# Optimization experiments

Measured on AMD Instinct MI355X. Metric: run time of the kernel, lower is better.

The kernel has to match this reference:

```python
import jax, jax.numpy as jnp
import numpy as np
import math


def setup_inputs() -> dict:
    B, L, D, P, V = 4, 4096, 512, 128, 8
    key = jax.random.key(0)
    ki = iter(jax.random.split(key, 40))
    def rn(shape, s=0.02):
        return jax.random.normal(next(ki), shape, jnp.float32) * s
    z = lambda *s: jnp.zeros(s, jnp.float32)
    return dict(
        x=jax.random.normal(next(ki), (B, L, D), jnp.float32),
        W_omega=rn((D, D)), b_omega=z(D),
        omega_scale=jnp.full((D,), 0.01, jnp.float32),
        W_pi1=rn((D, D)), b_pi1=z(D), W_pi2=rn((D, D)), b_pi2=z(D),
        W_m1v=rn((D, D)), b_m1v=z(D),
        W_m1o=rn((D, D)), b_m1o=z(D),
        W_mag=rn((D, D)), b_mag=z(D),
        mag_scale=jnp.asarray(5.0, jnp.float32),
        W_qoff=rn((D, D)), b_qoff=z(D),
        W_kenc=rn((D, P)), b_kenc=z(P),
        W_venc=rn((D, V)), b_venc=z(V),
        W_sk1=rn((2 * D, D)), b_sk1=z(D),
        W_sk2=rn((D, P)), b_sk2=z(P),
        W_sg=rn((D, 1)), b_sg=z(1),
        W_kvo=rn((V, D)), b_kvo=z(D),
        ln_g=jnp.ones((4 * D,), jnp.float32), ln_b=z(4 * D),
        W_o1=rn((4 * D, 2 * D)), b_o1=z(2 * D),
        W_o2=rn((2 * D, D)), b_o2=z(D),
    )


def _lin(h, W, b):
    return h @ W + b


def _gelu(h):
    return jax.nn.gelu(h, approximate=False)  # torch nn.GELU default (erf)


def _forward(x, W_omega, b_omega, omega_scale, W_pi1, b_pi1, W_pi2, b_pi2,
             W_m1v, b_m1v, W_m1o, b_m1o, W_mag, b_mag, mag_scale,
             W_qoff, b_qoff, W_kenc, b_kenc, W_venc, b_venc,
             W_sk1, b_sk1, W_sk2, b_sk2, W_sg, b_sg, W_kvo, b_kvo,
             ln_g, ln_b, W_o1, b_o1, W_o2, b_o2):
    B, L, D = x.shape
    P = W_kenc.shape[1]
    # --- evolving phases ---
    omega_scaled = _lin(x, W_omega, b_omega) * jnp.abs(omega_scale)
    phi_init = _lin(_gelu(_lin(x, W_pi1, b_pi1)), W_pi2, b_pi2)
    phi = phi_init + jnp.cumsum(omega_scaled, axis=1)
    cos_phi, sin_phi = jnp.cos(phi), jnp.sin(phi)
    # --- memory 1: positional phasor memory ---
    v1 = _lin(x, W_m1v, b_m1v)
    magnitude = jax.nn.sigmoid(_lin(x, W_mag, b_mag)) * jnp.abs(mag_scale)
    wv1 = magnitude * v1
    sqrt_mag = jnp.sqrt(jnp.cumsum(magnitude, axis=1) + 1e-8)
    mem1_cos = jnp.cumsum(wv1 * cos_phi, axis=1) / sqrt_mag
    mem1_sin = jnp.cumsum(wv1 * sin_phi, axis=1) / sqrt_mag
    phi_q = phi + _lin(x, W_qoff, b_qoff)
    pos_ret = (mem1_cos * jnp.cos(phi_q) + mem1_sin * jnp.sin(phi_q)) / math.sqrt(D)
    pos_out = _lin(pos_ret, W_m1o, b_m1o)
    # --- memory 2: key/value phasor binding ---
    query_phase = jnp.tanh(_lin(x, W_kenc, b_kenc)) * math.pi
    values = _lin(x, W_venc, b_venc)                      # [B,L,V]
    store_gate = jax.nn.sigmoid(_lin(x, W_sg, b_sg))      # [B,L,1]
    positions = jnp.arange(1, L + 1, dtype=x.dtype)[None, :, None]
    context_avg = jnp.cumsum(x, axis=1) / positions
    sk_in = jnp.concatenate([x, context_avg], axis=-1)
    storage_phase = jnp.tanh(_lin(_gelu(_lin(sk_in, W_sk1, b_sk1)), W_sk2, b_sk2)) * math.pi
    store_cos, store_sin = jnp.cos(storage_phase), jnp.sin(storage_phase)  # [B,L,P]
    gv = values * store_gate                               # [B,L,V]
    # [B,L,P,V] outer products, cumsum along L
    kv_mem_cos = jnp.cumsum(store_cos[..., None] * gv[:, :, None, :], axis=1)
    kv_mem_sin = jnp.cumsum(store_sin[..., None] * gv[:, :, None, :], axis=1)
    gate_cum = jnp.clip(jnp.cumsum(store_gate, axis=1), 1.0, None)  # [B,L,1]
    inv_norm = (1.0 / jnp.sqrt(gate_cum))[..., None]
    kv_mem_cos = kv_mem_cos * inv_norm
    kv_mem_sin = kv_mem_sin * inv_norm
    q_cos, q_sin = jnp.cos(query_phase), jnp.sin(query_phase)
    kv_retrieved = (jnp.einsum('blp,blpv->blv', q_cos, kv_mem_cos)
                    + jnp.einsum('blp,blpv->blv', q_sin, kv_mem_sin)) / math.sqrt(P)
    kv_out = _lin(kv_retrieved, W_kvo, b_kvo)
    # --- output projection ---
    combined = jnp.concatenate([pos_out, kv_out, x * cos_phi, x * sin_phi], axis=-1)
    mu = combined.mean(axis=-1, keepdims=True)
    var = combined.var(axis=-1, keepdims=True)
    h = (combined - mu) / jnp.sqrt(var + 1e-5) * ln_g + ln_b
    h = _gelu(_lin(h, W_o1, b_o1))  # dropout is identity in eval mode
    return x + _lin(h, W_o2, b_o2)


def reference(x, W_omega, b_omega, omega_scale, W_pi1, b_pi1, W_pi2, b_pi2,
              W_m1v, b_m1v, W_m1o, b_m1o, W_mag, b_mag, mag_scale,
              W_qoff, b_qoff, W_kenc, b_kenc, W_venc, b_venc,
              W_sk1, b_sk1, W_sk2, b_sk2, W_sg, b_sg, W_kvo, b_kvo,
              ln_g, ln_b, W_o1, b_o1, W_o2, b_o2):
    return _forward(x, W_omega, b_omega, omega_scale, W_pi1, b_pi1, W_pi2, b_pi2,
                    W_m1v, b_m1v, W_m1o, b_m1o, W_mag, b_mag, mag_scale,
                    W_qoff, b_qoff, W_kenc, b_kenc, W_venc, b_venc,
                    W_sk1, b_sk1, W_sk2, b_sk2, W_sg, b_sg, W_kvo, b_kvo,
                    ln_g, ln_b, W_o1, b_o1, W_o2, b_o2)
```

## Files before the change

### kernel.cpp

```cpp
#include <hip/hip_runtime.h>
#include <math.h>

#define B_ 4
#define L_ 4096
#define D_ 512
#define P_ 128
#define V_ 8
#define N_ (B_*L_)
#define NC 64
#define CL (L_/NC)
#define LD ((size_t)L_*D_)
#define PI_F 3.14159265358979323846f

typedef unsigned short ushort;
typedef __attribute__((ext_vector_type(8))) short bh8;
typedef __attribute__((ext_vector_type(4))) float f4;
typedef const __attribute__((address_space(1))) unsigned int gu32;
typedef __attribute__((address_space(3))) unsigned int lu32;

__device__ __forceinline__ float geluf(float v){
    return 0.5f*v*(1.0f+erff(v*0.7071067811865475f));
}
__device__ __forceinline__ float tanhf_fast(float x){
    return 1.0f - 2.0f/(__expf(2.0f*x)+1.0f);
}
__device__ __forceinline__ ushort f2b(float f){
    union { float f; unsigned u; } v; v.f = f;
    unsigned r = (v.u + 0x7fffu + ((v.u >> 16) & 1u)) >> 16;
    return (ushort)r;
}
__device__ __forceinline__ float b2f(ushort h){
    union { unsigned u; float f; } v; v.u = ((unsigned)h) << 16;
    return v.f;
}
__device__ __forceinline__ void gload16(const ushort* g, ushort* l){
    __builtin_amdgcn_global_load_lds((gu32*)g, (lu32*)l, 16, 0, 0);
}
__device__ __forceinline__ int xcd_swz(int orig, int nwg){
    int q8 = nwg >> 3, r8 = nwg & 7;
    int xcd = orig & 7, sub = orig >> 3;
    return (xcd < r8 ? xcd*(q8+1) : r8*(q8+1) + (xcd-r8)*q8) + sub;
}

template<int ACT>
__global__ __launch_bounds__(256, 2)
void dgemm_k(const ushort* __restrict__ A, int lda,
             const ushort* __restrict__ Wt, const float* __restrict__ bias,
             ushort* __restrict__ Ob, float* __restrict__ Of,
             int ldc, int K, const float* __restrict__ addbuf)
{
    __shared__ ushort lA[2][128*64];
    __shared__ ushort lB[2][128*64];
    const int tid = threadIdx.x, lane = tid & 63, w = tid >> 6;
    const int wr = w >> 1, wc = w & 1;
    const int nbx = gridDim.x;
    const int wg = xcd_swz(blockIdx.y*nbx + blockIdx.x, nbx*gridDim.y);
    const int row0 = (wg / nbx) * 128, col0 = (wg % nbx) * 128;

    f4 zero4 = {0.f,0.f,0.f,0.f};
    f4 acc[4][4];
    #pragma unroll
    for (int i=0;i<4;i++)
        #pragma unroll
        for (int j=0;j<4;j++) acc[i][j] = zero4;

    auto stage = [&](int buf, int kt){
        #pragma unroll
        for (int is=0; is<4; ++is){
            int id = tid + is*256;
            int r = id >> 3, p = id & 7;
            int srcc = (p ^ (r & 7)) * 8;
            gload16(A + (size_t)(row0 + r)*lda + kt + srcc, &lA[buf][r*64 + p*8]);
        }
        #pragma unroll
        for (int is=0; is<4; ++is){
            int id = tid + is*256;
            int r = id >> 3, p = id & 7;
            int srcc = (p ^ (r & 7)) * 8;
            gload16(Wt + (size_t)(col0 + r)*K + kt + srcc, &lB[buf][r*64 + p*8]);
        }
    };

    const int NT = K >> 6;
    stage(0, 0);
    for (int t2 = 0; t2 < NT; ++t2){
        int cur = t2 & 1;
        if (t2 + 1 < NT){
            stage(cur ^ 1, (t2+1) << 6);
            asm volatile("s_waitcnt vmcnt(8)" ::: "memory");
        } else {
            asm volatile("s_waitcnt vmcnt(0)" ::: "memory");
        }
        __builtin_amdgcn_s_barrier();
        __builtin_amdgcn_sched_barrier(0);
        #pragma unroll
        for (int h=0; h<2; ++h){
            bh8 af[4], bf_[4];
            #pragma unroll
            for (int i=0;i<4;i++){
                int row = wr*64 + i*16 + (lane & 15);
                int pc = (h*4 + (lane >> 4)) ^ (row & 7);
                af[i] = *(const bh8*)&lA[cur][row*64 + pc*8];
            }
            #pragma unroll
            for (int j=0;j<4;j++){
                int row = wc*64 + j*16 + (lane & 15);
                int pc = (h*4 + (lane >> 4)) ^ (row & 7);
                bf_[j] = *(const bh8*)&lB[cur][row*64 + pc*8];
            }
            #pragma unroll
            for (int i=0;i<4;i++)
                #pragma unroll
                for (int j=0;j<4;j++)
                    acc[i][j] = __builtin_amdgcn_mfma_f32_16x16x32_bf16(af[i], bf_[j], acc[i][j], 0, 0, 0);
        }
        __builtin_amdgcn_sched_barrier(0);
        __builtin_amdgcn_s_barrier();
    }

    #pragma unroll
    for (int i=0;i<4;i++){
        int rr = row0 + wr*64 + i*16 + ((lane >> 4) << 2);
        #pragma unroll
        for (int j=0;j<4;j++){
            int cc = col0 + wc*64 + j*16 + (lane & 15);
            float bv = bias[cc];
            #pragma unroll
            for (int q=0;q<4;q++){
                int r = rr + q;
                float t = acc[i][j][q] + bv;
                if (ACT==2){
                    if (addbuf) t += addbuf[(size_t)r*512 + cc];
                    Of[(size_t)r*ldc + cc] = t;
                } else {
                    if (ACT==1) t = geluf(t);
                    Ob[(size_t)r*ldc + cc] = f2b(t);
                }
            }
        }
    }
}

__global__ __launch_bounds__(256, 2)
void fgemm_k(const ushort* __restrict__ A, int lda, const ushort* __restrict__ Wt,
             const float* __restrict__ bs0, const float* __restrict__ bs1,
             const float* __restrict__ bs2, const float* __restrict__ bs3,
             const float* __restrict__ bs4, const float* __restrict__ bs5,
             ushort* __restrict__ o0, ushort* __restrict__ o1p, ushort* __restrict__ o2p,
             ushort* __restrict__ o3p, ushort* __restrict__ o4p,
             ushort* __restrict__ Qc, ushort* __restrict__ Qs,
             const float* __restrict__ omsc, const float* __restrict__ magscp, int K)
{
    __shared__ ushort lA[2][128*32];
    __shared__ ushort lB[2][128*32];
    const int tid = threadIdx.x, lane = tid & 63, w = tid >> 6;
    const int wr = w >> 1, wc = w & 1;
    const int nbx = gridDim.x;
    const int wg = xcd_swz(blockIdx.y*nbx + blockIdx.x, nbx*gridDim.y);
    const int row0 = (wg / nbx) * 128, col0 = (wg % nbx) * 128;

    const int srow = w*32 + (lane >> 2);
    const int sch  = lane & 3;
    const int scolA = (sch ^ (srow & 3)) * 8;
    const ushort* gA0 = A  + (size_t)(row0 + srow)      * lda + scolA;
    const ushort* gA1 = A  + (size_t)(row0 + srow + 16) * lda + scolA;
    const ushort* gB0 = Wt + (size_t)(col0 + srow)      * K   + scolA;
    const ushort* gB1 = Wt + (size_t)(col0 + srow + 16) * K   + scolA;
    const int d0 = srow*32 + sch*8, d1 = (srow+16)*32 + sch*8;

    f4 zero4 = {0.f,0.f,0.f,0.f};
    f4 acc[4][4];
    #pragma unroll
    for (int i=0;i<4;i++)
        #pragma unroll
        for (int j=0;j<4;j++) acc[i][j] = zero4;

    const int fr = lane & 15;
    const int pcr = (((lane >> 4) ^ (fr & 3))) * 8;
    gload16(gA0, &lA[0][d0]); gload16(gA1, &lA[0][d1]);
    gload16(gB0, &lB[0][d0]); gload16(gB1, &lB[0][d1]);
    __syncthreads();
    int cur = 0;
    for (int kt = 0; kt < K; kt += 32) {
        int nxt = cur ^ 1;
        if (kt + 32 < K) {
            gload16(gA0 + kt + 32, &lA[nxt][d0]); gload16(gA1 + kt + 32, &lA[nxt][d1]);
            gload16(gB0 + kt + 32, &lB[nxt][d0]); gload16(gB1 + kt + 32, &lB[nxt][d1]);
        }
        bh8 af[4], bfr[4];
        #pragma unroll
        for (int i=0;i<4;i++){
            af[i]  = *(const bh8*)&lA[cur][(wr*64 + i*16 + fr)*32 + pcr];
            bfr[i] = *(const bh8*)&lB[cur][(wc*64 + i*16 + fr)*32 + pcr];
        }
        #pragma unroll
        for (int i=0;i<4;i++)
            #pragma unroll
            for (int j=0;j<4;j++)
                acc[i][j] = __builtin_amdgcn_mfma_f32_16x16x32_bf16(af[i], bfr[j], acc[i][j], 0, 0, 0);
        __syncthreads();
        cur = nxt;
    }

    const int seg = col0 >> 9;
    if (seg == 5) {
        #pragma unroll
        for (int i=0;i<4;i++){
            int rr = row0 + wr*64 + i*16 + ((lane >> 4) << 2);
            #pragma unroll
            for (int j=0;j<4;j++){
                int lcc = (col0 - 2560) + wc*64 + j*16 + (lane & 15);
                float bv = bs5[lcc];
                #pragma unroll
                for (int q=0;q<4;q++){
                    int r = rr + q;
                    float ph = tanhf_fast(acc[i][j][q] + bv)*PI_F;
                    Qc[(size_t)r*128 + lcc] = f2b(__cosf(ph));
                    Qs[(size_t)r*128 + lcc] = f2b(__sinf(ph));
                }
            }
        }
        return;
    }
    const float* bias = seg==0?bs0: seg==1?bs1: seg==2?bs2: seg==3?bs3: bs4;
    ushort* dst = seg==0?o0: seg==1?o1p: seg==2?o2p: seg==3?o3p: o4p;
    float msc = fabsf(*magscp);
    #pragma unroll
    for (int i=0;i<4;i++){
        int rr = row0 + wr*64 + i*16 + ((lane >> 4) << 2);
        #pragma unroll
        for (int j=0;j<4;j++){
            int cc = col0 + wc*64 + j*16 + (lane & 15);
            int lcc = cc & 511;
            float bv = bias[lcc];
            float csc = (seg==0) ? fabsf(omsc[lcc]) : 1.0f;
            #pragma unroll
            for (int q=0;q<4;q++){
                int r = rr + q;
                float t = acc[i][j][q] + bv;
                if (seg==1)      t = msc/(1.0f+__expf(-t));
                else if (seg==3) t = geluf(t);
                else             t *= csc;
                dst[(size_t)r*512 + lcc] = f2b(t);
            }
        }
    }
}

__global__ __launch_bounds__(256, 2)
void mgemm_k(const ushort* __restrict__ Apos, const ushort* __restrict__ Ask,
             const ushort* __restrict__ Wm1o, const ushort* __restrict__ Wsk2,
             const float* __restrict__ bm1o, const float* __restrict__ bsk2,
             ushort* __restrict__ planes, ushort* __restrict__ Kc, ushort* __restrict__ Ks)
{
    __shared__ ushort lA[2][128*32];
    __shared__ ushort lB[2][128*32];
    const int tid = threadIdx.x, lane = tid & 63, w = tid >> 6;
    const int wr = w >> 1, wc = w & 1;
    const int nbx = gridDim.x;
    const int wg = xcd_swz(blockIdx.y*nbx + blockIdx.x, nbx*gridDim.y);
    const int row0 = (wg / nbx) * 128, col0 = (wg % nbx) * 128;
    const int seg = col0 >> 9;
    const ushort* A  = seg ? Ask  : Apos;
    const ushort* Wt = seg ? Wsk2 : Wm1o;
    const int wcol0 = seg ? (col0 - 512) : col0;
    const int K = 512;

    const int srow = w*32 + (lane >> 2);
    const int sch  = lane & 3;
    const int scolA = (sch ^ (srow & 3)) * 8;
    const ushort* gA0 = A  + (size_t)(row0 + srow)       * 512 + scolA;
    const ushort* gA1 = A  + (size_t)(row0 + srow + 16)  * 512 + scolA;
    const ushort* gB0 = Wt + (size_t)(wcol0 + srow)      * 512 + scolA;
    const ushort* gB1 = Wt + (size_t)(wcol0 + srow + 16) * 512 + scolA;
    const int d0 = srow*32 + sch*8, d1 = (srow+16)*32 + sch*8;

    f4 zero4 = {0.f,0.f,0.f,0.f};
    f4 acc[4][4];
    #pragma unroll
    for (int i=0;i<4;i++)
        #pragma unroll
        for (int j=0;j<4;j++) acc[i][j] = zero4;

    const int fr = lane & 15;
    const int pcr = (((lane >> 4) ^ (fr & 3))) * 8;
    gload16(gA0, &lA[0][d0]); gload16(gA1, &lA[0][d1]);
    gload16(gB0, &lB[0][d0]); gload16(gB1, &lB[0][d1]);
    __syncthreads();
    int cur = 0;
    for (int kt = 0; kt < K; kt += 32) {
        int nxt = cur ^ 1;
        if (kt + 32 < K) {
            gload16(gA0 + kt + 32, &lA[nxt][d0]); gload16(gA1 + kt + 32, &lA[nxt][d1]);
            gload16(gB0 + kt + 32, &lB[nxt][d0]); gload16(gB1 + kt + 32, &lB[nxt][d1]);
        }
        bh8 af[4], bfr[4];
        #pragma unroll
        for (int i=0;i<4;i++){
            af[i]  = *(const bh8*)&lA[cur][(wr*64 + i*16 + fr)*32 + pcr];
            bfr[i] = *(const bh8*)&lB[cur][(wc*64 + i*16 + fr)*32 + pcr];
        }
        #pragma unroll
        for (int i=0;i<4;i++)
            #pragma unroll
            for (int j=0;j<4;j++)
                acc[i][j] = __builtin_amdgcn_mfma_f32_16x16x32_bf16(af[i], bfr[j], acc[i][j], 0, 0, 0);
        __syncthreads();
        cur = nxt;
    }

    #pragma unroll
    for (int i=0;i<4;i++){
        int rr = row0 + wr*64 + i*16 + ((lane >> 4) << 2);
        #pragma unroll
        for (int j=0;j<4;j++){
            int cc = col0 + wc*64 + j*16 + (lane & 15);
            #pragma unroll
            for (int q=0;q<4;q++){
                int r = rr + q;
                if (seg == 0){
                    planes[(size_t)r*2048 + cc] = f2b(acc[i][j][q] + bm1o[cc]);
                } else {
                    int lcc = cc - 512;
                    float ph = tanhf_fast(acc[i][j][q] + bsk2[lcc])*PI_F;
                    Kc[(size_t)r*128 + lcc] = f2b(__cosf(ph));
                    Ks[(size_t)r*128 + lcc] = f2b(__sinf(ph));
                }
            }
        }
    }
}

struct WtArgs {
    const float* src[12];
    ushort* dst[12];
    int K[12], M[12], t0[13];
};
__global__ __launch_bounds__(256)
void wtall_k(WtArgs a)
{
    __shared__ float tile[32][33];
    int bb = blockIdx.x;
    int j = 0;
    while (bb >= a.t0[j+1]) ++j;
    int tt = bb - a.t0[j];
    int K = a.K[j], M = a.M[j];
    int mt = M >> 5;
    int kb = (tt / mt) * 32, mb = (tt % mt) * 32;
    const float* W = a.src[j]; ushort* Wt = a.dst[j];
    int tx = threadIdx.x & 31, ty = threadIdx.x >> 5;
    #pragma unroll
    for (int i = ty; i < 32; i += 8)
        tile[i][tx] = W[(size_t)(kb+i)*M + mb+tx];
    __syncthreads();
    #pragma unroll
    for (int i = ty; i < 32; i += 8)
        Wt[(size_t)(mb+i)*K + kb+tx] = f2b(tile[tx][i]);
}

__global__ __launch_bounds__(256)
void fconv_k(const float* __restrict__ in, ushort* __restrict__ xctx)
{
    size_t i = ((size_t)blockIdx.x*256 + threadIdx.x) * 4;
    size_t row = i >> 9; int d = (int)(i & 511);
    float4 v = *(const float4*)(in + i);
    ushort* o = xctx + row*1024 + d;
    o[0]=f2b(v.x); o[1]=f2b(v.y); o[2]=f2b(v.z); o[3]=f2b(v.w);
}

__global__ __launch_bounds__(256)
void s1a_k(const ushort* __restrict__ omega, const ushort* __restrict__ xctx,
           float* __restrict__ csA, float* __restrict__ csX)
{
    int bid = blockIdx.x;
    int b = bid >> 7; int rem = bid & 127;
    int dg = rem & 1, c = rem >> 1;
    int d = dg*256 + threadIdx.x;
    size_t row0 = (size_t)b*L_ + (size_t)c*CL;
    size_t base = row0*D_ + d;
    float sA=0.f, sX=0.f;
    for (int l=0;l<CL;l++){
        sA += b2f(omega[base + (size_t)l*D_]);
        sX += b2f(xctx[(row0 + l)*1024 + d]);
    }
    size_t ci = ((size_t)b*NC + c)*D_ + d;
    csA[ci]=sA; csX[ci]=sX;
}

__global__ __launch_bounds__(256)
void aux1_k(float* __restrict__ csA, float* __restrict__ csX,
            const float* __restrict__ sgate, float* __restrict__ rinv, int nb2)
{
    __shared__ float wsum[4];
    __shared__ float carry;
    int bb = blockIdx.x, t = threadIdx.x;
    if (bb < nb2){
        int tt = bb*256 + t;
        int b = tt >> 9, d = tt & 511;
        float* bufs[2] = {csA, csX};
        #pragma unroll
        for (int i=0;i<2;i++){
            float* p = bufs[i] + ((size_t)b*NC)*D_ + d;
            float run=0.f;
            for (int c=0;c<NC;c++){
                float v = p[(size_t)c*D_];
                p[(size_t)c*D_] = run;
                run += v;
            }
        }
        return;
    }
    int b = bb - nb2;
    int lane = t & 63, wave = t >> 6;
    if (t == 0) carry = 0.f;
    __syncthreads();
    for (int s = 0; s < L_/256; s++){
        float v = sgate[(size_t)b*L_ + s*256 + t];
        float sc = v;
        #pragma unroll
        for (int off=1; off<64; off<<=1){
            float u = __shfl_up(sc, off, 64);
            if (lane >= off) sc += u;
        }
        if (lane == 63) wsum[wave] = sc;
        __syncthreads();
        float woff = carry;
        for (int w2 = 0; w2 < wave; w2++) woff += wsum[w2];
        float inc = sc + woff;
        rinv[(size_t)b*L_ + s*256 + t] = rsqrtf(fmaxf(inc, 1.0f));
        __syncthreads();
        if (t == 255) carry = inc;
        __syncthreads();
    }
}

__global__ void prefix_k(float* a, float* b2v, float* c3, int nbuf)
{
    int t = blockIdx.x*blockDim.x + threadIdx.x;
    int b = t >> 9, d = t & 511;
    float* bufs[3] = {a,b2v,c3};
    for (int i=0;i<nbuf;i++){
        float* p = bufs[i] + ((size_t)b*NC)*D_ + d;
        float run=0.f;
        for (int c=0;c<NC;c++){
            float v = p[(size_t)c*D_];
            p[(size_t)c*D_] = run;
            run += v;
        }
    }
}

__global__ __launch_bounds__(256)
void s1c_k(const ushort* __restrict__ omega, const ushort* __restrict__ phi_init,
           const ushort* __restrict__ magn, const ushort* __restrict__ v1,
           const float* __restrict__ csA, const float* __restrict__ csX,
           ushort* __restrict__ cphi, ushort* __restrict__ sphi, ushort* __restrict__ xctx,
           float* __restrict__ csM, float* __restrict__ csC, float* __restrict__ csS)
{
    int bid = blockIdx.x;
    int b = bid >> 7; int rem = bid & 127;
    int dg = rem & 1, c = rem >> 1;
    int d = dg*256 + threadIdx.x;
    size_t ci = ((size_t)b*NC + c)*D_ + d;
    float phiacc = csA[ci], xacc = csX[ci];
    float sM=0.f,sC=0.f,sS=0.f;
    size_t xrow = (size_t)b*L_ + (size_t)c*CL;
    size_t base = xrow*D_ + d;
    for (int l=0;l<CL;l++){
        size_t idx = base + (size_t)l*D_;
        phiacc += b2f(omega[idx]);
        float ph = b2f(phi_init[idx]) + phiacc;
        float spv = __sinf(ph), cpv = __cosf(ph);
        cphi[idx] = f2b(cpv); sphi[idx] = f2b(spv);
        xacc += b2f(xctx[(xrow + l)*1024 + d]);
        xctx[(xrow + l)*1024 + 512 + d] = f2b(__fdividef(xacc, (float)(c*CL + l + 1)));
        float m = b2f(magn[idx]); sM += m;
        float wv = m * b2f(v1[idx]);
        sC = fmaf(wv, cpv, sC); sS = fmaf(wv, spv, sS);
    }
    csM[ci]=sM; csC[ci]=sC; csS[ci]=sS;
}

__global__ __launch_bounds__(256)
void s1e_k(const ushort* __restrict__ magn, const ushort* __restrict__ v1,
           const ushort* qoff, const ushort* __restrict__ cphi, const ushort* __restrict__ sphi,
           const float* __restrict__ csM, const float* __restrict__ csC,
           const float* __restrict__ csS, ushort* pos_ret)
{
    int bid = blockIdx.x;
    int b = bid >> 7; int rem = bid & 127;
    int dg = rem & 1, c = rem >> 1;
    int d = dg*256 + threadIdx.x;
    size_t ci = ((size_t)b*NC + c)*D_ + d;
    float mA=csM[ci], cA=csC[ci], sA=csS[ci];
    size_t base = ((size_t)b*L_ + (size_t)c*CL)*D_ + d;
    for (int l=0;l<CL;l++){
        size_t idx = base + (size_t)l*D_;
        float m = b2f(magn[idx]); mA += m;
        float wv = m * b2f(v1[idx]);
        float cp = b2f(cphi[idx]), sp = b2f(sphi[idx]);
        cA = fmaf(wv, cp, cA); sA = fmaf(wv, sp, sA);
        float rs = rsqrtf(mA + 1e-8f);
        float qo = b2f(qoff[idx]);
        float sq = __sinf(qo), cq = __cosf(qo);
        float cosq = cp*cq - sp*sq;
        float sinq = sp*cq + cp*sq;
        pos_ret[idx] = f2b((cA*cosq + sA*sinq) * rs * 0.04419417382415922f);
    }
}

__global__ __launch_bounds__(256)
void vencsg_k(const ushort* __restrict__ xctx, const float* __restrict__ Wv,
              const float* __restrict__ bv, const float* __restrict__ Wg,
              const float* __restrict__ bg,
              ushort* __restrict__ gvb, float* __restrict__ sgate)
{
    int gw = (int)((blockIdx.x*(size_t)blockDim.x + threadIdx.x) >> 6);
    int lane = threadIdx.x & 63;
    const ushort* xr = xctx + (size_t)gw*1024;
    float pv[8] = {0,0,0,0,0,0,0,0}; float pg = 0.f;
    #pragma unroll
    for (int j=0;j<8;j++){
        int k = lane + 64*j;
        float xv = b2f(xr[k]);
        #pragma unroll
        for (int v=0;v<8;v++) pv[v] = fmaf(xv, Wv[k*8+v], pv[v]);
        pg = fmaf(xv, Wg[k], pg);
    }
    #pragma unroll
    for (int off=32; off>0; off>>=1){
        #pragma unroll
        for (int v=0;v<8;v++) pv[v] += __shfl_down(pv[v], off, 64);
        pg += __shfl_down(pg, off, 64);
    }
    if (lane==0){
        float sg = 1.0f/(1.0f+__expf(-(pg + bg[0])));
        #pragma unroll
        for (int v=0;v<8;v++) gvb[(size_t)gw*8+v] = f2b((pv[v] + bv[v]) * sg);
        sgate[gw] = sg;
    }
}

__global__ __launch_bounds__(256)
void kvsum_k(const ushort* __restrict__ Kc, const ushort* __restrict__ Ks,
             const ushort* __restrict__ gvb, float* __restrict__ csKV)
{
    int bid = blockIdx.x;
    int b = bid >> 6, c = bid & 63;
    int t = threadIdx.x; int p = t & 127; int v0 = (t>>7)*4;
    size_t row0 = (size_t)b*L_ + (size_t)c*64;
    float ac[4]={0,0,0,0}, as[4]={0,0,0,0};
    for (int l=0;l<64;l++){
        size_t r = row0 + l;
        float kc = b2f(Kc[r*(size_t)P_ + p]);
        float ks = b2f(Ks[r*(size_t)P_ + p]);
        #pragma unroll
        for (int j=0;j<4;j++){
            float gv = b2f(gvb[r*(size_t)V_ + v0 + j]);
            ac[j] = fmaf(kc, gv, ac[j]);
            as[j] = fmaf(ks, gv, as[j]);
        }
    }
    float* base = csKV + ((size_t)b*64 + c)*2048;
    #pragma unroll
    for (int j=0;j<4;j++){
        base[p*V_ + v0 + j] = ac[j];
        base[1024 + p*V_ + v0 + j] = as[j];
    }
}

__global__ void kvpfx_k(float* __restrict__ csKV)
{
    int t = blockIdx.x*blockDim.x + threadIdx.x;
    int b = t >> 11, si = t & 2047;
    float* ptr = csKV + ((size_t)b*64)*2048 + si;
    float run=0.f;
    for (int c=0;c<64;c++){
        float v = ptr[(size_t)c*2048];
        ptr[(size_t)c*2048] = run;
        run += v;
    }
}

__global__ __launch_bounds__(256)
void kv2_k(const ushort* __restrict__ Qc, const ushort* __restrict__ Qs,
           const ushort* __restrict__ Kc, const ushort* __restrict__ Ks,
           const ushort* __restrict__ gvb, const float* __restrict__ rinv,
           const float* __restrict__ csKV, float* __restrict__ kvret)
{
    __shared__ ushort sS[64][66];
    __shared__ float sM[2048];
    __shared__ float sgv[64][8];
    int tile = blockIdx.x, b = blockIdx.y;
    int t = threadIdx.x, lane = t & 63, w = t >> 6;
    int wr = w >> 1, wc = w & 1;
    size_t row0 = (size_t)b*L_ + (size_t)tile*64;
    const float* kvb = csKV + ((size_t)b*64 + tile)*2048;
    #pragma unroll
    for (int k=0;k<8;k++) sM[t + k*256] = kvb[t + k*256];
    #pragma unroll
    for (int k=0;k<2;k++){
        int idx = t + k*256; int l = idx >> 3, v = idx & 7;
        sgv[l][v] = b2f(gvb[(row0 + l)*(size_t)V_ + v]);
    }
    f4 zero4 = {0.f,0.f,0.f,0.f};
    f4 acc[2][2];
    #pragma unroll
    for (int i=0;i<2;i++)
        #pragma unroll
        for (int j=0;j<2;j++) acc[i][j] = zero4;
    #pragma unroll
    for (int ks=0; ks<8; ks++){
        const ushort* Ab = (ks<4) ? Qc : Qs;
        const ushort* Bb = (ks<4) ? Kc : Ks;
        int kb = (ks&3)*32 + (lane>>4)*8;
        bh8 af[2], bfr[2];
        #pragma unroll
        for (int i=0;i<2;i++)
            af[i] = *(const bh8*)(Ab + (row0 + wr*32 + i*16 + (lane&15))*(size_t)P_ + kb);
        #pragma unroll
        for (int j=0;j<2;j++)
            bfr[j] = *(const bh8*)(Bb + (row0 + wc*32 + j*16 + (lane&15))*(size_t)P_ + kb);
        #pragma unroll
        for (int i=0;i<2;i++)
            #pragma unroll
            for (int j=0;j<2;j++)
                acc[i][j] = __builtin_amdgcn_mfma_f32_16x16x32_bf16(af[i], bfr[j], acc[i][j], 0, 0, 0);
    }
    #pragma unroll
    for (int i=0;i<2;i++){
        #pragma unroll
        for (int j=0;j<2;j++){
            int cc = wc*32 + j*16 + (lane & 15);
            #pragma unroll
            for (int q=0;q<4;q++){
                int lr = wr*32 + i*16 + ((lane>>4)<<2) + q;
                sS[lr][cc] = f2b((cc <= lr) ? acc[i][j][q] : 0.f);
            }
        }
    }
    __syncthreads();
    int l = t & 63, vh = t >> 6; int v0 = vh*2;
    const ushort* qcr = Qc + (row0 + l)*(size_t)P_;
    const ushort* qsr = Qs + (row0 + l)*(size_t)P_;
    float a0=0.f, a1=0.f;
    #pragma unroll
    for (int pc=0; pc<16; pc++){
        bh8 qc8 = *(const bh8*)(qcr + pc*8);
        bh8 qs8 = *(const bh8*)(qsr + pc*8);
        #pragma unroll
        for (int e=0;e<8;e++){
            int p = pc*8+e;
            float qc = b2f((ushort)qc8[e]), qs = b2f((ushort)qs8[e]);
            a0 += qc*sM[p*8+v0]   + qs*sM[1024+p*8+v0];
            a1 += qc*sM[p*8+v0+1] + qs*sM[1024+p*8+v0+1];
        }
    }
    for (int c=0;c<64;c++){
        float sv = b2f(sS[l][c]);
        a0 = fmaf(sv, sgv[c][v0],   a0);
        a1 = fmaf(sv, sgv[c][v0+1], a1);
    }
    float rn = rinv[row0 + l] * 0.08838834764831845f;
    kvret[(row0+l)*(size_t)V_ + v0]   = a0*rn;
    kvret[(row0+l)*(size_t)V_ + v0+1] = a1*rn;
}

__global__ __launch_bounds__(256)
void cmb_k(const ushort* __restrict__ xctx, const ushort* __restrict__ cphi,
           const ushort* __restrict__ sphi,
           const float* __restrict__ kvret, const float* __restrict__ Wkvo,
           const float* __restrict__ bkvo,
           const float* __restrict__ ln_g, const float* __restrict__ ln_b,
           ushort* pl)
{
    __shared__ float red[8];
    __shared__ float kvv[8];
    int n = blockIdx.x; int t = threadIdx.x;
    int wave = t>>6, lane = t&63;
    if (t < 8) kvv[t] = kvret[(size_t)n*8 + t];
    __syncthreads();
    float v_[8]; float sum=0.f, sumsq=0.f;
    #pragma unroll
    for (int i=0;i<8;i++){
        int cidx = t + i*256;
        int seg = cidx >> 9, cc = cidx & 511;
        float v;
        if (seg == 0) v = b2f(pl[(size_t)n*2048 + cidx]);
        else if (seg == 1) {
            v = bkvo[cc];
            #pragma unroll
            for (int vv=0; vv<8; vv++) v = fmaf(kvv[vv], Wkvo[vv*512 + cc], v);
        } else {
            size_t id = (size_t)n*D_ + cc;
            v = b2f(xctx[(size_t)n*1024 + cc]) * b2f((seg==2) ? cphi[id] : sphi[id]);
        }
        v_[i]=v; sum += v; sumsq = fmaf(v,v,sumsq);
    }
    #pragma unroll
    for (int off=32; off>0; off>>=1){
        sum += __shfl_xor(sum, off, 64);
        sumsq += __shfl_xor(sumsq, off, 64);
    }
    if (lane==0){ red[wave]=sum; red[wave+4]=sumsq; }
    __syncthreads();
    float s = red[0]+red[1]+red[2]+red[3];
    float q = red[4]+red[5]+red[6]+red[7];
    float mu = s * (1.0f/2048.0f);
    float var = q * (1.0f/2048.0f) - mu*mu;
    float rstd = rsqrtf(var + 1e-5f);
    #pragma unroll
    for (int i=0;i<8;i++){
        int cidx = t + i*256;
        float h = (v_[i]-mu)*rstd*ln_g[cidx] + ln_b[cidx];
        pl[(size_t)n*2048 + cidx] = f2b(h);
    }
}

__global__ void copyx_k(const float* __restrict__ x, float* __restrict__ out, size_t n)
{
    size_t i = (size_t)blockIdx.x*256 + threadIdx.x;
    if (i < n) out[i] = x[i];
}

struct WS {
    ushort *wt_fused,*wt_pi2,*wt_sk1,*wt_sk2,*wt_m1o,*wt_o1,*wt_o2;
    ushort *xctx, *pool;
    ushort *Qc,*Qs,*Kc,*Ks,*gvb,*cphi,*sphi;
    float *sgate,*rinv,*kvret;
    float *csA,*csX,*csM,*csC,*csS,*csKV;
};

static size_t ws_layout(WS& w, char* base, int NB)
{
    size_t off = 0;
    auto al = [&](size_t bytes)->char* {
        char* p = base + off; off = (off + bytes + 255) & ~(size_t)255; return p;
    };
    size_t R = (size_t)NB * L_;
    w.wt_fused=(ushort*)al((size_t)2688*512*2);
    w.wt_pi2 =(ushort*)al(512*512*2);
    w.wt_sk1 =(ushort*)al((size_t)512*1024*2); w.wt_sk2=(ushort*)al(128*512*2);
    w.wt_m1o =(ushort*)al(512*512*2);
    w.wt_o1  =(ushort*)al((size_t)1024*2048*2); w.wt_o2=(ushort*)al((size_t)512*1024*2);
    w.xctx=(ushort*)al(R*1024*2);
    w.pool=(ushort*)al(R*512*2*6);
    w.Qc=(ushort*)al(R*128*2); w.Qs=(ushort*)al(R*128*2);
    w.Kc=(ushort*)al(R*128*2); w.Ks=(ushort*)al(R*128*2);
    w.gvb=(ushort*)al(R*8*2);
    w.cphi=(ushort*)al(R*512*2); w.sphi=(ushort*)al(R*512*2);
    w.sgate=(float*)al(R*4); w.rinv=(float*)al(R*4); w.kvret=(float*)al(R*8*4);
    w.csA=(float*)al((size_t)NB*NC*512*4); w.csX=(float*)al((size_t)NB*NC*512*4);
    w.csM=(float*)al((size_t)NB*NC*512*4); w.csC=(float*)al((size_t)NB*NC*512*4);
    w.csS=(float*)al((size_t)NB*NC*512*4);
    w.csKV=(float*)al((size_t)NB*64*2048*4);
    return off;
}

extern "C" void kernel_launch(void* const* d_in, const int* in_sizes, int n_in,
                              void* d_out, int out_size, void* d_ws, size_t ws_size,
                              hipStream_t stream)
{
    const float* x        =(const float*)d_in[0];
    const float* W_omega  =(const float*)d_in[1];  const float* b_omega=(const float*)d_in[2];
    const float* omega_sc =(const float*)d_in[3];
    const float* W_pi1    =(const float*)d_in[4];  const float* b_pi1 =(const float*)d_in[5];
    const float* W_pi2    =(const float*)d_in[6];  const float* b_pi2 =(const float*)d_in[7];
    const float* W_m1v    =(const float*)d_in[8];  const float* b_m1v =(const float*)d_in[9];
    const float* W_m1o    =(const float*)d_in[10]; const float* b_m1o =(const float*)d_in[11];
    const float* W_mag    =(const float*)d_in[12]; const float* b_mag =(const float*)d_in[13];
    const float* mag_sc   =(const float*)d_in[14];
    const float* W_qoff   =(const float*)d_in[15]; const float* b_qoff=(const float*)d_in[16];
    const float* W_kenc   =(const float*)d_in[17]; const float* b_kenc=(const float*)d_in[18];
    const float* W_venc   =(const float*)d_in[19]; const float* b_venc=(const float*)d_in[20];
    const float* W_sk1    =(const float*)d_in[21]; const float* b_sk1 =(const float*)d_in[22];
    const float* W_sk2    =(const float*)d_in[23]; const float* b_sk2 =(const float*)d_in[24];
    const float* W_sg     =(const float*)d_in[25]; const float* b_sg  =(const float*)d_in[26];
    const float* W_kvo    =(const float*)d_in[27]; const float* b_kvo =(const float*)d_in[28];
    const float* ln_g     =(const float*)d_in[29]; const float* ln_b  =(const float*)d_in[30];
    const float* W_o1     =(const float*)d_in[31]; const float* b_o1  =(const float*)d_in[32];
    const float* W_o2     =(const float*)d_in[33]; const float* b_o2  =(const float*)d_in[34];
    float* out = (float*)d_out;

    char* wsb = (char*)d_ws;
    WS w;
    int NB = 4;
    if (ws_layout(w, wsb, 4) > ws_size) {
        NB = 2;
        if (ws_layout(w, wsb, 2) > ws_size) {
            NB = 1;
            if (ws_layout(w, wsb, 1) > ws_size) {
                copyx_k<<<dim3((unsigned)(((size_t)N_*D_ + 255)/256)), dim3(256), 0, stream>>>(x, out, (size_t)N_*D_);
                return;
            }
        }
    }

    dim3 blk(256);
    WtArgs wa;
    const float* srcs[12] = {W_omega, W_mag, W_m1v, W_pi1, W_qoff, W_kenc,
                             W_pi2, W_sk1, W_sk2, W_m1o, W_o1, W_o2};
    ushort* dsts[12] = {w.wt_fused + (size_t)0*512*512, w.wt_fused + (size_t)1*512*512,
                        w.wt_fused + (size_t)2*512*512, w.wt_fused + (size_t)3*512*512,
                        w.wt_fused + (size_t)4*512*512, w.wt_fused + (size_t)5*512*512,
                        w.wt_pi2, w.wt_sk1, w.wt_sk2, w.wt_m1o, w.wt_o1, w.wt_o2};
    int Ks_[12] = {512,512,512,512,512,512, 512,1024,512,512,2048,1024};
    int Ms_[12] = {512,512,512,512,512,128, 512, 512,128,512,1024, 512};
    int cum = 0;
    for (int j = 0; j < 12; ++j){
        wa.src[j]=srcs[j]; wa.dst[j]=dsts[j]; wa.K[j]=Ks_[j]; wa.M[j]=Ms_[j];
        wa.t0[j]=cum; cum += (Ks_[j]/32)*(Ms_[j]/32);
    }
    wa.t0[12]=cum;
    wtall_k<<<dim3(cum), blk, 0, stream>>>(wa);

    const int R = NB * L_;
    const size_t SL = (size_t)R * 512;
    ushort* bA = w.pool;        ushort* bB = w.pool + SL;
    ushort* bC = w.pool + 2*SL; ushort* bD = w.pool + 3*SL;
    ushort* bE = w.pool + 4*SL; ushort* bF = w.pool + 5*SL;
    ushort* planes = w.pool;
    ushort* h1 = w.pool + 4*SL;

    #define DGEMM(ACT,A,lda,Wt_,bias_,Ob_,Of_,ldc,K_,M_,add_) \
        dgemm_k<ACT><<<dim3((M_)/128, R/128), blk, 0, stream>>>(A,lda,Wt_,bias_,Ob_,Of_,ldc,K_,add_)

    for (int g = 0; g < B_/NB; ++g) {
        const float* xg = x + (size_t)g*NB*LD;
        float* outg = out + (size_t)g*NB*LD;

        fconv_k<<<dim3((unsigned)((size_t)R*512/1024)), blk, 0, stream>>>(xg, w.xctx);

        fgemm_k<<<dim3(2688/128, R/128), blk, 0, stream>>>(
            w.xctx,1024, w.wt_fused, b_omega,b_mag,b_m1v,b_pi1,b_qoff,b_kenc,
            bA,bB,bC,bD,bF, w.Qc,w.Qs, omega_sc, mag_sc, 512);
        DGEMM(0, bD,512, w.wt_pi2, b_pi2, bE,(float*)0, 512, 512,512, (const float*)0);
        vencsg_k<<<dim3((unsigned)((size_t)R*64/256)), blk, 0, stream>>>(w.xctx, W_venc,b_venc, W_sg,b_sg, w.gvb, w.sgate);
        s1a_k<<<dim3(NB*NC*2), blk, 0, stream>>>(bA, w.xctx, w.csA, w.csX);
        aux1_k<<<dim3(NB*2 + NB), blk, 0, stream>>>(w.csA, w.csX, w.sgate, w.rinv, NB*2);
        s1c_k<<<dim3(NB*NC*2), blk, 0, stream>>>(bA, bE, bB, bC, w.csA, w.csX,
                                                 w.cphi, w.sphi, w.xctx, w.csM, w.csC, w.csS);
        prefix_k<<<dim3(NB*2), blk, 0, stream>>>(w.csM, w.csC, w.csS, 3);
        s1e_k<<<dim3(NB*NC*2), blk, 0, stream>>>(bB, bC, bF, w.cphi, w.sphi,
                                                 w.csM, w.csC, w.csS, bF);

        DGEMM(1, w.xctx,1024, w.wt_sk1, b_sk1, bE,(float*)0, 512, 1024,512, (const float*)0);
        mgemm_k<<<dim3(640/128, R/128), blk, 0, stream>>>(
            bF, bE, w.wt_m1o, w.wt_sk2, b_m1o, b_sk2, planes, w.Kc, w.Ks);

        kvsum_k<<<dim3(NB*64), blk, 0, stream>>>(w.Kc, w.Ks, w.gvb, w.csKV);
        kvpfx_k<<<dim3(NB*8), blk, 0, stream>>>(w.csKV);
        kv2_k<<<dim3(64, NB), blk, 0, stream>>>(w.Qc, w.Qs, w.Kc, w.Ks, w.gvb, w.rinv, w.csKV, w.kvret);

        cmb_k<<<dim3(R), blk, 0, stream>>>(w.xctx, w.cphi, w.sphi, w.kvret, W_kvo, b_kvo,
                                           ln_g, ln_b, planes);
        DGEMM(1, planes,2048, w.wt_o1, b_o1, h1,(float*)0, 1024, 2048,1024, (const float*)0);
        DGEMM(2, h1,1024, w.wt_o2, b_o2, (ushort*)0,outg, 512, 1024,512, xg);
    }
    #undef DGEMM
}
```

Baseline: 476.1 us.

## Add 256x256-tile GEMM for W_o1 and fuse x column sums into conversion

Adds a 512-thread GEMM kernel with 256x256 tiles, eight waves, double-buffered LDS and raised wave priority, and uses it for the largest projection (K=2048, M=1024). The larger tile raises data reuse per load and cuts global traffic, at the cost of fewer workgroups and more register and LDS pressure. The bf16 conversion of x now also computes the per-chunk column sums of x, so s1a no longer rereads xctx. The serial chunk-prefix scans in aux1 and prefix_k are split across more blocks, one buffer per block, to add parallelism.

Measured after the change: 476.3 us. Within noise of the previous version (+0.0%).

```diff
diff --git a/kernel.cpp b/kernel.cpp
--- a/kernel.cpp
+++ b/kernel.cpp
@@ -121,6 +121,107 @@
     #pragma unroll
     for (int i=0;i<4;i++){
         int rr = row0 + wr*64 + i*16 + ((lane >> 4) << 2);
+        #pragma unroll
+        for (int j=0;j<4;j++){
+            int cc = col0 + wc*64 + j*16 + (lane & 15);
+            float bv = bias[cc];
+            #pragma unroll
+            for (int q=0;q<4;q++){
+                int r = rr + q;
+                float t = acc[i][j][q] + bv;
+                if (ACT==2){
+                    if (addbuf) t += addbuf[(size_t)r*512 + cc];
+                    Of[(size_t)r*ldc + cc] = t;
+                } else {
+                    if (ACT==1) t = geluf(t);
+                    Ob[(size_t)r*ldc + cc] = f2b(t);
+                }
+            }
+        }
+    }
+}
+
+template<int ACT>
+__global__ __launch_bounds__(512, 1)
+void egemm_k(const ushort* __restrict__ A, int lda,
+             const ushort* __restrict__ Wt, const float* __restrict__ bias,
+             ushort* __restrict__ Ob, float* __restrict__ Of,
+             int ldc, int K, const float* __restrict__ addbuf)
+{
+    __shared__ ushort lA[2][256*64];
+    __shared__ ushort lB[2][256*64];
+    const int tid = threadIdx.x, lane = tid & 63, w = tid >> 6;
+    const int wr = w >> 2, wc = w & 3;
+    const int nbx = gridDim.x;
+    const int wg = xcd_swz(blockIdx.y*nbx + blockIdx.x, nbx*gridDim.y);
+    const int row0 = (wg / nbx) * 256, col0 = (wg % nbx) * 256;
+
+    f4 zero4 = {0.f,0.f,0.f,0.f};
+    f4 acc[8][4];
+    #pragma unroll
+    for (int i=0;i<8;i++)
+        #pragma unroll
+        for (int j=0;j<4;j++) acc[i][j] = zero4;
+
+    auto stage = [&](int buf, int kt){
+        #pragma unroll
+        for (int is=0; is<4; ++is){
+            int id = tid + is*512;
+            int r = id >> 3, p = id & 7;
+            int srcc = (p ^ (r & 7)) * 8;
+            gload16(A + (size_t)(row0 + r)*lda + kt + srcc, &lA[buf][r*64 + p*8]);
+        }
+        #pragma unroll
+        for (int is=0; is<4; ++is){
+            int id = tid + is*512;
+            int r = id >> 3, p = id & 7;
+            int srcc = (p ^ (r & 7)) * 8;
+            gload16(Wt + (size_t)(col0 + r)*K + kt + srcc, &lB[buf][r*64 + p*8]);
+        }
+    };
+
+    const int NT = K >> 6;
+    stage(0, 0);
+    for (int t2 = 0; t2 < NT; ++t2){
+        int cur = t2 & 1;
+        if (t2 + 1 < NT){
+            stage(cur ^ 1, (t2+1) << 6);
+            asm volatile("s_waitcnt vmcnt(8)" ::: "memory");
+        } else {
+            asm volatile("s_waitcnt vmcnt(0)" ::: "memory");
+        }
+        __builtin_amdgcn_s_barrier();
+        __builtin_amdgcn_sched_barrier(0);
+        __builtin_amdgcn_s_setprio(1);
+        #pragma unroll
+        for (int h=0; h<2; ++h){
+            bh8 af[8], bf_[4];
+            #pragma unroll
+            for (int i=0;i<8;i++){
+                int row = wr*128 + i*16 + (lane & 15);
+                int pc = (h*4 + (lane >> 4)) ^ (row & 7);
+                af[i] = *(const bh8*)&lA[cur][row*64 + pc*8];
+            }
+            #pragma unroll
+            for (int j=0;j<4;j++){
+                int row = wc*64 + j*16 + (lane & 15);
+                int pc = (h*4 + (lane >> 4)) ^ (row & 7);
+                bf_[j] = *(const bh8*)&lB[cur][row*64 + pc*8];
+            }
+            #pragma unroll
+            for (int i=0;i<8;i++)
+                #pragma unroll
+                for (int j=0;j<4;j++)
+                    acc[i][j] = __builtin_amdgcn_mfma_f32_16x16x32_bf16(af[i], bf_[j], acc[i][j], 0, 0, 0);
+        }
+        __builtin_amdgcn_s_setprio(0);
+        __builtin_amdgcn_sched_barrier(0);
+        __builtin_amdgcn_s_barrier();
+    }
+
+    #pragma unroll
+    for (int i=0;i<8;i++){
+        int rr = row0 + wr*128 + i*16 + ((lane >> 4) << 2);
         #pragma unroll
         for (int j=0;j<4;j++){
             int cc = col0 + wc*64 + j*16 + (lane & 15);
@@ -359,32 +460,35 @@
 }
 
 __global__ __launch_bounds__(256)
-void fconv_k(const float* __restrict__ in, ushort* __restrict__ xctx)
-{
-    size_t i = ((size_t)blockIdx.x*256 + threadIdx.x) * 4;
-    size_t row = i >> 9; int d = (int)(i & 511);
-    float4 v = *(const float4*)(in + i);
-    ushort* o = xctx + row*1024 + d;
-    o[0]=f2b(v.x); o[1]=f2b(v.y); o[2]=f2b(v.z); o[3]=f2b(v.w);
+void fconv_k(const float* __restrict__ in, ushort* __restrict__ xctx,
+             float* __restrict__ csX)
+{
+    int bc = blockIdx.x;
+    int t = threadIdx.x;
+    int d = t*2;
+    size_t row0 = (size_t)bc * CL;
+    float s0=0.f, s1=0.f;
+    for (int l=0;l<CL;l++){
+        float2 v = *(const float2*)(in + (row0+l)*D_ + d);
+        ushort h0 = f2b(v.x), h1 = f2b(v.y);
+        xctx[(row0+l)*1024 + d]   = h0;
+        xctx[(row0+l)*1024 + d+1] = h1;
+        s0 += b2f(h0); s1 += b2f(h1);
+    }
+    csX[(size_t)bc*512 + d]   = s0;
+    csX[(size_t)bc*512 + d+1] = s1;
 }
 
 __global__ __launch_bounds__(256)
-void s1a_k(const ushort* __restrict__ omega, const ushort* __restrict__ xctx,
-           float* __restrict__ csA, float* __restrict__ csX)
+void s1a_k(const ushort* __restrict__ omega, float* __restrict__ csA)
 {
     int bid = blockIdx.x;
-    int b = bid >> 7; int rem = bid & 127;
-    int dg = rem & 1, c = rem >> 1;
+    int bc = bid >> 1, dg = bid & 1;
     int d = dg*256 + threadIdx.x;
-    size_t row0 = (size_t)b*L_ + (size_t)c*CL;
-    size_t base = row0*D_ + d;
-    float sA=0.f, sX=0.f;
-    for (int l=0;l<CL;l++){
-        sA += b2f(omega[base + (size_t)l*D_]);
-        sX += b2f(xctx[(row0 + l)*1024 + d]);
-    }
-    size_t ci = ((size_t)b*NC + c)*D_ + d;
-    csA[ci]=sA; csX[ci]=sX;
+    size_t base = ((size_t)bc*CL)*D_ + d;
+    float sA=0.f;
+    for (int l=0;l<CL;l++) sA += b2f(omega[base + (size_t)l*D_]);
+    csA[(size_t)bc*D_ + d] = sA;
 }
 
 __global__ __launch_bounds__(256)
@@ -394,23 +498,21 @@
     __shared__ float wsum[4];
     __shared__ float carry;
     int bb = blockIdx.x, t = threadIdx.x;
-    if (bb < nb2){
-        int tt = bb*256 + t;
+    if (bb < 2*nb2){
+        float* buf = (bb < nb2) ? csA : csX;
+        int gb = (bb < nb2) ? bb : bb - nb2;
+        int tt = gb*256 + t;
         int b = tt >> 9, d = tt & 511;
-        float* bufs[2] = {csA, csX};
-        #pragma unroll
-        for (int i=0;i<2;i++){
-            float* p = bufs[i] + ((size_t)b*NC)*D_ + d;
-            float run=0.f;
-            for (int c=0;c<NC;c++){
-                float v = p[(size_t)c*D_];
-                p[(size_t)c*D_] = run;
-                run += v;
-            }
+        float* p = buf + ((size_t)b*NC)*D_ + d;
+        float run=0.f;
+        for (int c=0;c<NC;c++){
+            float v = p[(size_t)c*D_];
+            p[(size_t)c*D_] = run;
+            run += v;
         }
         return;
     }
-    int b = bb - nb2;
+    int b = bb - 2*nb2;
     int lane = t & 63, wave = t >> 6;
     if (t == 0) carry = 0.f;
     __syncthreads();
@@ -434,19 +536,20 @@
     }
 }
 
-__global__ void prefix_k(float* a, float* b2v, float* c3, int nbuf)
-{
-    int t = blockIdx.x*blockDim.x + threadIdx.x;
-    int b = t >> 9, d = t & 511;
+__global__ void prefix_k(float* a, float* b2v, float* c3, int nb2)
+{
+    int bb = blockIdx.x;
     float* bufs[3] = {a,b2v,c3};
-    for (int i=0;i<nbuf;i++){
-        float* p = bufs[i] + ((size_t)b*NC)*D_ + d;
-        float run=0.f;
-        for (int c=0;c<NC;c++){
-            float v = p[(size_t)c*D_];
-            p[(size_t)c*D_] = run;
-            run += v;
-        }
+    float* buf = bufs[bb / nb2];
+    int gb = bb % nb2;
+    int tt = gb*256 + threadIdx.x;
+    int b = tt >> 9, d = tt & 511;
+    float* p = buf + ((size_t)b*NC)*D_ + d;
+    float run=0.f;
+    for (int c=0;c<NC;c++){
+        float v = p[(size_t)c*D_];
+        p[(size_t)c*D_] = run;
+        run += v;
     }
 }
 
@@ -824,23 +927,25 @@
 
     #define DGEMM(ACT,A,lda,Wt_,bias_,Ob_,Of_,ldc,K_,M_,add_) \
         dgemm_k<ACT><<<dim3((M_)/128, R/128), blk, 0, stream>>>(A,lda,Wt_,bias_,Ob_,Of_,ldc,K_,add_)
+    #define EGEMM(ACT,A,lda,Wt_,bias_,Ob_,Of_,ldc,K_,M_,add_) \
+        egemm_k<ACT><<<dim3((M_)/256, R/256), dim3(512), 0, stream>>>(A,lda,Wt_,bias_,Ob_,Of_,ldc,K_,add_)
 
     for (int g = 0; g < B_/NB; ++g) {
         const float* xg = x + (size_t)g*NB*LD;
         float* outg = out + (size_t)g*NB*LD;
 
-        fconv_k<<<dim3((unsigned)((size_t)R*512/1024)), blk, 0, stream>>>(xg, w.xctx);
+        fconv_k<<<dim3(NB*NC), blk, 0, stream>>>(xg, w.xctx, w.csX);
 
         fgemm_k<<<dim3(2688/128, R/128), blk, 0, stream>>>(
             w.xctx,1024, w.wt_fused, b_omega,b_mag,b_m1v,b_pi1,b_qoff,b_kenc,
             bA,bB,bC,bD,bF, w.Qc,w.Qs, omega_sc, mag_sc, 512);
         DGEMM(0, bD,512, w.wt_pi2, b_pi2, bE,(float*)0, 512, 512,512, (const float*)0);
         vencsg_k<<<dim3((unsigned)((size_t)R*64/256)), blk, 0, stream>>>(w.xctx, W_venc,b_venc, W_sg,b_sg, w.gvb, w.sgate);
-        s1a_k<<<dim3(NB*NC*2), blk, 0, stream>>>(bA, w.xctx, w.csA, w.csX);
-        aux1_k<<<dim3(NB*2 + NB), blk, 0, stream>>>(w.csA, w.csX, w.sgate, w.rinv, NB*2);
+        s1a_k<<<dim3(NB*NC*2), blk, 0, stream>>>(bA, w.csA);
+        aux1_k<<<dim3(NB*4 + NB), blk, 0, stream>>>(w.csA, w.csX, w.sgate, w.rinv, NB*2);
         s1c_k<<<dim3(NB*NC*2), blk, 0, stream>>>(bA, bE, bB, bC, w.csA, w.csX,
                                                  w.cphi, w.sphi, w.xctx, w.csM, w.csC, w.csS);
-        prefix_k<<<dim3(NB*2), blk, 0, stream>>>(w.csM, w.csC, w.csS, 3);
+        prefix_k<<<dim3(NB*6), blk, 0, stream>>>(w.csM, w.csC, w.csS, NB*2);
         s1e_k<<<dim3(NB*NC*2), blk, 0, stream>>>(bB, bC, bF, w.cphi, w.sphi,
                                                  w.csM, w.csC, w.csS, bF);
 
@@ -854,8 +959,9 @@
 
         cmb_k<<<dim3(R), blk, 0, stream>>>(w.xctx, w.cphi, w.sphi, w.kvret, W_kvo, b_kvo,
                                            ln_g, ln_b, planes);
-        DGEMM(1, planes,2048, w.wt_o1, b_o1, h1,(float*)0, 1024, 2048,1024, (const float*)0);
+        EGEMM(1, planes,2048, w.wt_o1, b_o1, h1,(float*)0, 1024, 2048,1024, (const float*)0);
         DGEMM(2, h1,1024, w.wt_o2, b_o2, (ushort*)0,outg, 512, 1024,512, xg);
     }
     #undef DGEMM
-}
+    #undef EGEMM
+}
```
